# Kernel tuning notes

Measured on AMD Instinct MI355X. Metric: run time of the kernel, lower is better.

## Reference

```python
import jax, jax.numpy as jnp
import numpy as np

BETA = 0.25  # commitment-loss weight (kwargs['beta'])


def setup_inputs() -> dict:
    key = jax.random.key(0)
    k1, k2 = jax.random.split(key)
    B, C, H, W = 16, 256, 64, 64
    K = 2048
    feats = jax.random.normal(k1, (B, C, H, W), dtype=jnp.float32)
    # nn.Embedding init: uniform(-1/n_codewords, 1/codeword_dim)
    codebook = jax.random.uniform(k2, (K, C), minval=-1.0 / K, maxval=1.0 / C,
                                  dtype=jnp.float32)
    return {"feats": feats, "codebook": codebook}


def reference(feats, codebook):
    B, C, H, W = feats.shape
    K = codebook.shape[0]
    z = jnp.transpose(feats, (0, 2, 3, 1))          # [B,H,W,C]
    zf = z.reshape(-1, C)                            # [N,C], N=B*H*W
    # squared-euclidean distances via ||z||^2 + ||e||^2 - 2 z.e : [N,K]
    d = (jnp.sum(zf * zf, axis=1, keepdims=True)
         + jnp.sum(codebook * codebook, axis=1)
         - 2.0 * (zf @ codebook.T))
    min_encoding_indices = jnp.argmin(d, axis=1)     # [N]
    mat_id_probs = jax.nn.softmax(-jnp.abs(d), axis=1)  # [N,K]
    z_q = codebook[min_encoding_indices].reshape(z.shape)  # [B,H,W,C]
    loss = (BETA * jnp.mean((jax.lax.stop_gradient(z_q) - z) ** 2)
            + jnp.mean((z_q - jax.lax.stop_gradient(z)) ** 2))
    # straight-through estimator
    z_q_st = z + jax.lax.stop_gradient(z_q - z)
    z_q_out = jnp.transpose(z_q_st, (0, 3, 1, 2))    # [B,C,H,W]
    idx_out = min_encoding_indices.reshape(B, H, W)
    probs_out = jnp.transpose(mat_id_probs.reshape(B, H, W, K), (0, 3, 1, 2))
    return z_q_out, idx_out, loss, probs_out
```

## Files before the change

### kernel.cpp

```cpp
#include <hip/hip_runtime.h>

#define HW 4096
#define CC 256
#define KK 2048
#define BB 16
#define NN (BB*HW)
#define RPB 128

#define ZQ_SZ   (BB*CC*HW)
#define IDX_OFF ZQ_SZ
#define LOSS_OFF (IDX_OFF + NN)
#define PROBS_OFF (LOSS_OFF + 1)

#define EH_OFF 0
#define EE_OFF 262144
#define ZZ_OFF 264192

#define TAU 0.01f
#define CAND_CAP 512
#define KTC 64
#define KT_N 32

typedef short bf16x8 __attribute__((ext_vector_type(8)));
typedef float f32x16 __attribute__((ext_vector_type(16)));
typedef unsigned int u32;

__device__ __forceinline__ void gload16(const void* g, void* l){
  __builtin_amdgcn_global_load_lds(
      (const __attribute__((address_space(1))) u32*)g,
      (__attribute__((address_space(3))) u32*)l, 16, 0, 0);
}

__device__ __forceinline__ unsigned short bf16rn(float x){
  unsigned u = __float_as_uint(x);
  return (unsigned short)((u + 0x7fffu + ((u >> 16) & 1u)) >> 16);
}

template<int STRIDE>
__device__ __forceinline__ float np_sumsq256(const float* __restrict__ a){
  float res0 = 0.f, res1 = 0.f;
  #pragma unroll
  for (int h = 0; h < 2; h++){
    const float* p = a + (size_t)h * 128 * STRIDE;
    float r[8];
    #pragma unroll
    for (int j = 0; j < 8; j++){ float x = p[(size_t)j * STRIDE]; r[j] = __fmul_rn(x, x); }
    for (int i = 8; i < 128; i += 8){
      #pragma unroll
      for (int j = 0; j < 8; j++){
        float x = p[(size_t)(i + j) * STRIDE];
        r[j] = __fadd_rn(r[j], __fmul_rn(x, x));
      }
    }
    float s = __fadd_rn(__fadd_rn(__fadd_rn(r[0], r[1]), __fadd_rn(r[2], r[3])),
                        __fadd_rn(__fadd_rn(r[4], r[5]), __fadd_rn(r[6], r[7])));
    if (h == 0) res0 = s; else res1 = s;
  }
  return __fadd_rn(res0, res1);
}

__global__ void k_prep2(const float* __restrict__ cb, float* __restrict__ out){
  const int k = blockIdx.x * 256 + threadIdx.x;
  unsigned short* eh = (unsigned short*)(out + EH_OFF);
  const float* row = cb + (size_t)k * CC;
  for (int c = 0; c < CC; c++) eh[k * CC + c] = bf16rn(row[c]);
  out[EE_OFF + k] = np_sumsq256<1>(row);
}

__global__ void k_zz(const float* __restrict__ feats, float* __restrict__ out){
  const int n = blockIdx.x * 256 + threadIdx.x;
  const int b = n >> 12, hw = n & 4095;
  out[ZZ_OFF + n] = np_sumsq256<HW>(feats + (size_t)b * CC * HW + hw);
}

__global__ __launch_bounds__(256, 2)
void k_mfma(const float* __restrict__ feats, const float* __restrict__ cb,
            float* __restrict__ out){
  __shared__ __align__(16) unsigned char lds_e[2][32768];
  __shared__ float ee_lds[KK];
  __shared__ unsigned long long rowkey[RPB];
  __shared__ int cand[CAND_CAP];
  __shared__ int cand_n;
  __shared__ float lsum;

  const int t = threadIdx.x;
  const int w = t >> 6, l = t & 63;
  const int grp = l >> 5;
  const int lane31 = l & 31;
  const int n0 = blockIdx.x * RPB;
  const int bi = n0 >> 12;
  const int hw0 = n0 & 4095;
  const int myhw = hw0 + w * 32 + lane31;

  for (int i = t; i < KK; i += 256) ee_lds[i] = out[EE_OFF + i];
  if (t < RPB) rowkey[t] = ~0ull;
  if (t == 0){ cand_n = 0; lsum = 0.f; }

  bf16x8 ah0[16];
  {
    const float* zb = feats + (size_t)bi * CC * HW + myhw;
    #pragma unroll
    for (int cs = 0; cs < 16; ++cs){
      #pragma unroll
      for (int j = 0; j < 8; ++j)
        ah0[cs][j] = (short)bf16rn(zb[(size_t)(cs * 16 + grp * 8 + j) * HW]);
    }
  }

  const unsigned short* ehg = (const unsigned short*)(out + EH_OFF);

  int ofs_[8];
  #pragma unroll
  for (int i = 0; i < 8; ++i){
    int ix = i * 256 + t;
    int cd = ix & 63, g = (ix >> 6) & 1, cs = ix >> 7;
    ofs_[i] = cd * CC + cs * 16 + g * 8;
  }

#define STAGE(KT, B) { \
    const unsigned short* tb_ = ehg + (size_t)(KT) * (KTC * CC); \
    _Pragma("unroll") \
    for (int i_ = 0; i_ < 8; ++i_) \
      gload16(tb_ + ofs_[i_], &lds_e[B][(i_ * 256 + t) * 16]); }

#define COMPUTE(B) { \
    _Pragma("unroll") \
    for (int ii = 0; ii < 16; ++ii){ accA[ii] = 0.f; accB[ii] = 0.f; } \
    _Pragma("unroll") \
    for (int cs = 0; cs < 16; ++cs){ \
      const unsigned char* bp_ = &lds_e[B][(size_t)(cs * 2 + grp) * 1024 + lane31 * 16]; \
      bf16x8 e0_ = *(const bf16x8*)(bp_); \
      bf16x8 e1_ = *(const bf16x8*)(bp_ + 512); \
      accA = __builtin_amdgcn_mfma_f32_32x32x16_bf16(e0_, ah0[cs], accA, 0, 0, 0); \
      accB = __builtin_amdgcn_mfma_f32_32x32x16_bf16(e1_, ah0[cs], accB, 0, 0, 0); \
    } }

  f32x16 accA, accB;
  float m0 = 3e38f, ss0 = 0.f, inv0 = 0.f;

  STAGE(0, 0);
  __syncthreads();

  for (int kt = 0; kt < 2 * KT_N; ++kt){
    const int tt = kt & 31;
    const int buf = kt & 1;
    if (kt < 2 * KT_N - 1) STAGE((kt + 1) & 31, buf ^ 1);
    COMPUTE(buf);
    const int eebase = tt * 64 + 4 * grp;
    if (kt < KT_N){
      #pragma unroll
      for (int r = 0; r < 16; ++r){
        int off = (r & 3) + 8 * (r >> 2);
        float s0 = ee_lds[eebase + off]      - 2.f * accA[r];
        float s1 = ee_lds[eebase + off + 32] - 2.f * accB[r];
        m0 = fminf(m0, fminf(s0, s1));
        ss0 += __expf(-s0) + __expf(-s1);
      }
      if (kt == KT_N - 1){
        m0 = fminf(m0, __shfl_xor(m0, 32));
        ss0 += __shfl_xor(ss0, 32);
        inv0 = 1.f / ss0;
      }
    } else {
      float* pb = out + (size_t)PROBS_OFF
                + (size_t)(bi * KK + eebase) * HW + myhw;
      #pragma unroll
      for (int r = 0; r < 16; ++r){
        int off = (r & 3) + 8 * (r >> 2);
        float s0 = ee_lds[eebase + off]      - 2.f * accA[r];
        float s1 = ee_lds[eebase + off + 32] - 2.f * accB[r];
        float* p = pb + (size_t)off * HW;
        p[0]               = __expf(-s0) * inv0;
        p[(size_t)32 * HW] = __expf(-s1) * inv0;
        int cg = eebase + off;
        if (s0 <= m0 + TAU){
          int sl = atomicAdd(&cand_n, 1);
          if (sl < CAND_CAP) cand[sl] = ((w * 32 + lane31) << 16) | cg;
        }
        if (s1 <= m0 + TAU){
          int sl = atomicAdd(&cand_n, 1);
          if (sl < CAND_CAP) cand[sl] = ((w * 32 + lane31) << 16) | (cg + 32);
        }
      }
    }
    __syncthreads();
  }

  int nc = cand_n; if (nc > CAND_CAP) nc = CAND_CAP;
  for (int i = t; i < nc; i += 256){
    int rc = cand[i];
    int rl = rc >> 16, code = rc & 0xffff;
    int n = n0 + rl;
    const float* zp = feats + (size_t)(n >> 12) * CC * HW + (n & 4095);
    const float* ep = cb + (size_t)code * CC;
    float a = 0.f;
    #pragma unroll 8
    for (int c = 0; c < CC; ++c) a = __builtin_fmaf(zp[(size_t)c * HW], ep[c], a);
    float t1 = __fadd_rn(out[ZZ_OFF + n], ee_lds[code]);
    float d = __fadd_rn(t1, -2.f * a);
    unsigned long long key = ((unsigned long long)__float_as_uint(d) << 32) | (unsigned)code;
    atomicMin(&rowkey[rl], key);
  }
  __syncthreads();

  if (t < RPB) out[IDX_OFF + n0 + t] = (float)(int)(rowkey[t] & 0xffffffffu);

  if (t < RPB){
    int code = (int)(rowkey[t] & 0xffffffffu);
    const float* ep = cb + (size_t)code * CC;
    const float* zp = feats + (size_t)bi * CC * HW + hw0 + t;
    float s = 0.f;
    for (int c = 0; c < CC; ++c){
      float dz = ep[c] - zp[(size_t)c * HW];
      s = __builtin_fmaf(dz, dz, s);
    }
    atomicAdd(&lsum, s);
  }
  __syncthreads();
  if (t == 0) atomicAdd(out + LOSS_OFF, lsum * (1.25f / 16777216.f));
}

__global__ void k_zq(const float* __restrict__ cb, float* __restrict__ out){
  const int f4 = blockIdx.x * 256 + threadIdx.x;
  const int f = f4 * 4;
  const int b = f >> 20;
  const int rem = f & 1048575;
  const int c = rem >> 12;
  const int hw = rem & 4095;
  const int n = b * HW + hw;
  const float* idxf = out + IDX_OFF;
  float4 iv = *(const float4*)(idxf + n);
  float4 o;
  o.x = cb[(size_t)((int)iv.x) * CC + c];
  o.y = cb[(size_t)((int)iv.y) * CC + c];
  o.z = cb[(size_t)((int)iv.z) * CC + c];
  o.w = cb[(size_t)((int)iv.w) * CC + c];
  *(float4*)(out + f) = o;
}

extern "C" void kernel_launch(void* const* d_in, const int* in_sizes, int n_in,
                              void* d_out, int out_size, void* d_ws, size_t ws_size,
                              hipStream_t stream){
  const float* feats = (const float*)d_in[0];
  const float* cb    = (const float*)d_in[1];
  float* out = (float*)d_out;

  (void)hipMemsetAsync(out + LOSS_OFF, 0, sizeof(float), stream);
  hipLaunchKernelGGL(k_prep2, dim3(8),     dim3(256), 0, stream, cb, out);
  hipLaunchKernelGGL(k_zz,    dim3(256),   dim3(256), 0, stream, feats, out);
  hipLaunchKernelGGL(k_mfma,  dim3(512),   dim3(256), 0, stream, feats, cb, out);
  hipLaunchKernelGGL(k_zq,    dim3(16384), dim3(256), 0, stream, cb, out);
}
```

Measured before the change: 488.8 us.

## Fold codebook norms into MFMA via augmented K-slice, halve tile, raise occupancy

Precomputes -0.5*||e||^2 as a bf16 extra column and appends a 17th MFMA step with a ones vector, so the distance offset comes out of the matrix accumulator instead of being added from an LDS table. The code tile is halved to 32 codes, so each tile now splits its channel range across two accumulators that are summed at the end. The LDS footprint shrinks and launch bounds go from 2 to 4 blocks per CU to raise occupancy. The trade-offs are bf16 rounding of the norm term, which can shift softmax values and candidate selection, twice as many loop iterations each with its own barrier, and register pressure under the tighter launch bound.

New measurement: 534.8 us. 1.09x slower.

```diff
diff --git a/kernel.cpp b/kernel.cpp
--- a/kernel.cpp
+++ b/kernel.cpp
@@ -14,12 +14,14 @@
 
 #define EH_OFF 0
 #define EE_OFF 262144
-#define ZZ_OFF 264192
+#define EXT_OFF 264192
+#define ZZ_OFF 280576
 
 #define TAU 0.01f
 #define CAND_CAP 512
-#define KTC 64
-#define KT_N 32
+#define KTC 32
+#define KT_N 64
+#define CS_N 17
 
 typedef short bf16x8 __attribute__((ext_vector_type(8)));
 typedef float f32x16 __attribute__((ext_vector_type(16)));
@@ -62,9 +64,14 @@
 __global__ void k_prep2(const float* __restrict__ cb, float* __restrict__ out){
   const int k = blockIdx.x * 256 + threadIdx.x;
   unsigned short* eh = (unsigned short*)(out + EH_OFF);
+  unsigned short* ex = (unsigned short*)(out + EXT_OFF);
   const float* row = cb + (size_t)k * CC;
   for (int c = 0; c < CC; c++) eh[k * CC + c] = bf16rn(row[c]);
-  out[EE_OFF + k] = np_sumsq256<1>(row);
+  float ee = np_sumsq256<1>(row);
+  out[EE_OFF + k] = ee;
+  ex[k * 16] = bf16rn(-0.5f * ee);
+  #pragma unroll
+  for (int j = 1; j < 16; ++j) ex[k * 16 + j] = 0;
 }
 
 __global__ void k_zz(const float* __restrict__ feats, float* __restrict__ out){
@@ -73,11 +80,10 @@
   out[ZZ_OFF + n] = np_sumsq256<HW>(feats + (size_t)b * CC * HW + hw);
 }
 
-__global__ __launch_bounds__(256, 2)
+__global__ __launch_bounds__(256, 4)
 void k_mfma(const float* __restrict__ feats, const float* __restrict__ cb,
             float* __restrict__ out){
-  __shared__ __align__(16) unsigned char lds_e[2][32768];
-  __shared__ float ee_lds[KK];
+  __shared__ __align__(16) unsigned char lds_e[2][CS_N * 2 * KTC * 16];
   __shared__ unsigned long long rowkey[RPB];
   __shared__ int cand[CAND_CAP];
   __shared__ int cand_n;
@@ -92,11 +98,10 @@
   const int hw0 = n0 & 4095;
   const int myhw = hw0 + w * 32 + lane31;
 
-  for (int i = t; i < KK; i += 256) ee_lds[i] = out[EE_OFF + i];
   if (t < RPB) rowkey[t] = ~0ull;
   if (t == 0){ cand_n = 0; lsum = 0.f; }
 
-  bf16x8 ah0[16];
+  bf16x8 ah0[16], ahx;
   {
     const float* zb = feats + (size_t)bi * CC * HW + myhw;
     #pragma unroll
@@ -105,34 +110,47 @@
       for (int j = 0; j < 8; ++j)
         ah0[cs][j] = (short)bf16rn(zb[(size_t)(cs * 16 + grp * 8 + j) * HW]);
     }
+    #pragma unroll
+    for (int j = 0; j < 8; ++j) ahx[j] = 0;
+    if (grp == 0) ahx[0] = (short)0x3F80;
   }
 
   const unsigned short* ehg = (const unsigned short*)(out + EH_OFF);
-
-  int ofs_[8];
+  const unsigned short* exg = (const unsigned short*)(out + EXT_OFF);
+
+  int ofs_[4];
   #pragma unroll
-  for (int i = 0; i < 8; ++i){
+  for (int i = 0; i < 4; ++i){
     int ix = i * 256 + t;
-    int cd = ix & 63, g = (ix >> 6) & 1, cs = ix >> 7;
+    int cd = ix & 31, g = (ix >> 5) & 1, cs = ix >> 6;
     ofs_[i] = cd * CC + cs * 16 + g * 8;
   }
 
 #define STAGE(KT, B) { \
     const unsigned short* tb_ = ehg + (size_t)(KT) * (KTC * CC); \
     _Pragma("unroll") \
-    for (int i_ = 0; i_ < 8; ++i_) \
-      gload16(tb_ + ofs_[i_], &lds_e[B][(i_ * 256 + t) * 16]); }
+    for (int i_ = 0; i_ < 4; ++i_) \
+      gload16(tb_ + ofs_[i_], &lds_e[B][(i_ * 256 + t) * 16]); \
+    if (t < 64){ \
+      int cd_ = t & 31, g_ = (t >> 5) & 1; \
+      gload16(exg + ((size_t)((KT) * KTC + cd_) * 16 + g_ * 8), \
+              &lds_e[B][(1024 + t) * 16]); \
+    } }
 
 #define COMPUTE(B) { \
     _Pragma("unroll") \
     for (int ii = 0; ii < 16; ++ii){ accA[ii] = 0.f; accB[ii] = 0.f; } \
     _Pragma("unroll") \
     for (int cs = 0; cs < 16; ++cs){ \
-      const unsigned char* bp_ = &lds_e[B][(size_t)(cs * 2 + grp) * 1024 + lane31 * 16]; \
-      bf16x8 e0_ = *(const bf16x8*)(bp_); \
-      bf16x8 e1_ = *(const bf16x8*)(bp_ + 512); \
-      accA = __builtin_amdgcn_mfma_f32_32x32x16_bf16(e0_, ah0[cs], accA, 0, 0, 0); \
-      accB = __builtin_amdgcn_mfma_f32_32x32x16_bf16(e1_, ah0[cs], accB, 0, 0, 0); \
+      const unsigned char* bp_ = &lds_e[B][(size_t)(cs * 2 + grp) * 512 + lane31 * 16]; \
+      bf16x8 e_ = *(const bf16x8*)(bp_); \
+      if (cs & 1) accB = __builtin_amdgcn_mfma_f32_32x32x16_bf16(e_, ah0[cs], accB, 0, 0, 0); \
+      else        accA = __builtin_amdgcn_mfma_f32_32x32x16_bf16(e_, ah0[cs], accA, 0, 0, 0); \
+    } \
+    { \
+      const unsigned char* bp_ = &lds_e[B][(size_t)(16 * 2 + grp) * 512 + lane31 * 16]; \
+      bf16x8 e_ = *(const bf16x8*)(bp_); \
+      accA = __builtin_amdgcn_mfma_f32_32x32x16_bf16(e_, ahx, accA, 0, 0, 0); \
     } }
 
   f32x16 accA, accB;
@@ -142,19 +160,16 @@
   __syncthreads();
 
   for (int kt = 0; kt < 2 * KT_N; ++kt){
-    const int tt = kt & 31;
+    const int tt = kt & 63;
     const int buf = kt & 1;
-    if (kt < 2 * KT_N - 1) STAGE((kt + 1) & 31, buf ^ 1);
+    if (kt < 2 * KT_N - 1) STAGE((kt + 1) & 63, buf ^ 1);
     COMPUTE(buf);
-    const int eebase = tt * 64 + 4 * grp;
     if (kt < KT_N){
       #pragma unroll
       for (int r = 0; r < 16; ++r){
-        int off = (r & 3) + 8 * (r >> 2);
-        float s0 = ee_lds[eebase + off]      - 2.f * accA[r];
-        float s1 = ee_lds[eebase + off + 32] - 2.f * accB[r];
-        m0 = fminf(m0, fminf(s0, s1));
-        ss0 += __expf(-s0) + __expf(-s1);
+        float s = -2.f * (accA[r] + accB[r]);
+        m0 = fminf(m0, s);
+        ss0 += __expf(-s);
       }
       if (kt == KT_N - 1){
         m0 = fminf(m0, __shfl_xor(m0, 32));
@@ -163,23 +178,16 @@
       }
     } else {
       float* pb = out + (size_t)PROBS_OFF
-                + (size_t)(bi * KK + eebase) * HW + myhw;
+                + (size_t)(bi * KK + tt * KTC + 4 * grp) * HW + myhw;
       #pragma unroll
       for (int r = 0; r < 16; ++r){
         int off = (r & 3) + 8 * (r >> 2);
-        float s0 = ee_lds[eebase + off]      - 2.f * accA[r];
-        float s1 = ee_lds[eebase + off + 32] - 2.f * accB[r];
-        float* p = pb + (size_t)off * HW;
-        p[0]               = __expf(-s0) * inv0;
-        p[(size_t)32 * HW] = __expf(-s1) * inv0;
-        int cg = eebase + off;
-        if (s0 <= m0 + TAU){
+        float s = -2.f * (accA[r] + accB[r]);
+        pb[(size_t)off * HW] = __expf(-s) * inv0;
+        if (s <= m0 + TAU){
           int sl = atomicAdd(&cand_n, 1);
-          if (sl < CAND_CAP) cand[sl] = ((w * 32 + lane31) << 16) | cg;
-        }
-        if (s1 <= m0 + TAU){
-          int sl = atomicAdd(&cand_n, 1);
-          if (sl < CAND_CAP) cand[sl] = ((w * 32 + lane31) << 16) | (cg + 32);
+          if (sl < CAND_CAP)
+            cand[sl] = ((w * 32 + lane31) << 16) | (tt * KTC + 4 * grp + off);
         }
       }
     }
@@ -196,7 +204,7 @@
     float a = 0.f;
     #pragma unroll 8
     for (int c = 0; c < CC; ++c) a = __builtin_fmaf(zp[(size_t)c * HW], ep[c], a);
-    float t1 = __fadd_rn(out[ZZ_OFF + n], ee_lds[code]);
+    float t1 = __fadd_rn(out[ZZ_OFF + n], out[EE_OFF + code]);
     float d = __fadd_rn(t1, -2.f * a);
     unsigned long long key = ((unsigned long long)__float_as_uint(d) << 32) | (unsigned)code;
     atomicMin(&rowkey[rl], key);
```

## Software-pipeline MFMA loop with ping-pong accumulators; parallelize codebook bf16 conversion

Applied to the files above, without the earlier changes.

The main loop is unrolled by two, with two accumulator sets, so the exp and probability-store post-processing of the previous tile runs alongside the MFMAs of the current tile. The codebook bf16 conversion moves from 8 blocks of 2048 serial threads to 256 blocks doing vectorized 16-byte writes. The separate ||z||^2 kernel is removed, and the norm is now computed only for candidate rows during refinement. The cost is more register pressure from the extra accumulators and repeated strided feature reads for each candidate.

After: 460.6 us (median of 2 runs). 5.8% less time.

```diff
diff --git a/kernel.cpp b/kernel.cpp
--- a/kernel.cpp
+++ b/kernel.cpp
@@ -14,7 +14,6 @@
 
 #define EH_OFF 0
 #define EE_OFF 262144
-#define ZZ_OFF 264192
 
 #define TAU 0.01f
 #define CAND_CAP 512
@@ -24,6 +23,7 @@
 typedef short bf16x8 __attribute__((ext_vector_type(8)));
 typedef float f32x16 __attribute__((ext_vector_type(16)));
 typedef unsigned int u32;
+typedef unsigned long long u64;
 
 __device__ __forceinline__ void gload16(const void* g, void* l){
   __builtin_amdgcn_global_load_lds(
@@ -59,18 +59,19 @@
   return __fadd_rn(res0, res1);
 }
 
-__global__ void k_prep2(const float* __restrict__ cb, float* __restrict__ out){
+__global__ void k_cvt(const float* __restrict__ cb, float* __restrict__ out){
+  const int i = blockIdx.x * 256 + threadIdx.x;
+  const int k = i >> 5, c8 = (i & 31) * 8;
+  const float* row = cb + (size_t)k * CC + c8;
+  unsigned short v[8];
+  #pragma unroll
+  for (int j = 0; j < 8; ++j) v[j] = bf16rn(row[j]);
+  *(uint4*)((unsigned short*)(out + EH_OFF) + (size_t)k * CC + c8) = *(uint4*)v;
+}
+
+__global__ void k_ee(const float* __restrict__ cb, float* __restrict__ out){
   const int k = blockIdx.x * 256 + threadIdx.x;
-  unsigned short* eh = (unsigned short*)(out + EH_OFF);
-  const float* row = cb + (size_t)k * CC;
-  for (int c = 0; c < CC; c++) eh[k * CC + c] = bf16rn(row[c]);
-  out[EE_OFF + k] = np_sumsq256<1>(row);
-}
-
-__global__ void k_zz(const float* __restrict__ feats, float* __restrict__ out){
-  const int n = blockIdx.x * 256 + threadIdx.x;
-  const int b = n >> 12, hw = n & 4095;
-  out[ZZ_OFF + n] = np_sumsq256<HW>(feats + (size_t)b * CC * HW + hw);
+  out[EE_OFF + k] = np_sumsq256<1>(cb + (size_t)k * CC);
 }
 
 __global__ __launch_bounds__(256, 2)
@@ -123,90 +124,105 @@
     for (int i_ = 0; i_ < 8; ++i_) \
       gload16(tb_ + ofs_[i_], &lds_e[B][(i_ * 256 + t) * 16]); }
 
-#define COMPUTE(B) { \
+#define COMPUTE(B, AA, AB) { \
     _Pragma("unroll") \
-    for (int ii = 0; ii < 16; ++ii){ accA[ii] = 0.f; accB[ii] = 0.f; } \
+    for (int ii = 0; ii < 16; ++ii){ AA[ii] = 0.f; AB[ii] = 0.f; } \
     _Pragma("unroll") \
     for (int cs = 0; cs < 16; ++cs){ \
       const unsigned char* bp_ = &lds_e[B][(size_t)(cs * 2 + grp) * 1024 + lane31 * 16]; \
       bf16x8 e0_ = *(const bf16x8*)(bp_); \
       bf16x8 e1_ = *(const bf16x8*)(bp_ + 512); \
-      accA = __builtin_amdgcn_mfma_f32_32x32x16_bf16(e0_, ah0[cs], accA, 0, 0, 0); \
-      accB = __builtin_amdgcn_mfma_f32_32x32x16_bf16(e1_, ah0[cs], accB, 0, 0, 0); \
+      AA = __builtin_amdgcn_mfma_f32_32x32x16_bf16(e0_, ah0[cs], AA, 0, 0, 0); \
+      AB = __builtin_amdgcn_mfma_f32_32x32x16_bf16(e1_, ah0[cs], AB, 0, 0, 0); \
     } }
 
-  f32x16 accA, accB;
+#define POST(PKT, PA, PB_) { \
+    const int ptt = (PKT) & 31; \
+    const int eebase = ptt * 64 + 4 * grp; \
+    if ((PKT) < KT_N){ \
+      _Pragma("unroll") \
+      for (int r = 0; r < 16; ++r){ \
+        int off = (r & 3) + 8 * (r >> 2); \
+        float s0 = ee_lds[eebase + off]      - 2.f * PA[r]; \
+        float s1 = ee_lds[eebase + off + 32] - 2.f * PB_[r]; \
+        m0 = fminf(m0, fminf(s0, s1)); \
+        ss0 += __expf(-s0) + __expf(-s1); \
+      } \
+    } else { \
+      float* pb = out + (size_t)PROBS_OFF \
+                + (size_t)(bi * KK + ptt * 64 + 4 * grp) * HW + myhw; \
+      _Pragma("unroll") \
+      for (int r = 0; r < 16; ++r){ \
+        int off = (r & 3) + 8 * (r >> 2); \
+        float s0 = ee_lds[eebase + off]      - 2.f * PA[r]; \
+        float s1 = ee_lds[eebase + off + 32] - 2.f * PB_[r]; \
+        float* p = pb + (size_t)off * HW; \
+        p[0]               = __expf(-s0) * inv0; \
+        p[(size_t)32 * HW] = __expf(-s1) * inv0; \
+        int cg = eebase + off; \
+        if (s0 <= m0 + TAU){ \
+          int sl = atomicAdd(&cand_n, 1); \
+          if (sl < CAND_CAP) cand[sl] = ((w * 32 + lane31) << 16) | cg; \
+        } \
+        if (s1 <= m0 + TAU){ \
+          int sl = atomicAdd(&cand_n, 1); \
+          if (sl < CAND_CAP) cand[sl] = ((w * 32 + lane31) << 16) | (cg + 32); \
+        } \
+      } \
+    } }
+
+  f32x16 aA0, aB0, aA1, aB1;
   float m0 = 3e38f, ss0 = 0.f, inv0 = 0.f;
 
   STAGE(0, 0);
   __syncthreads();
 
-  for (int kt = 0; kt < 2 * KT_N; ++kt){
-    const int tt = kt & 31;
-    const int buf = kt & 1;
-    if (kt < 2 * KT_N - 1) STAGE((kt + 1) & 31, buf ^ 1);
-    COMPUTE(buf);
-    const int eebase = tt * 64 + 4 * grp;
-    if (kt < KT_N){
-      #pragma unroll
-      for (int r = 0; r < 16; ++r){
-        int off = (r & 3) + 8 * (r >> 2);
-        float s0 = ee_lds[eebase + off]      - 2.f * accA[r];
-        float s1 = ee_lds[eebase + off + 32] - 2.f * accB[r];
-        m0 = fminf(m0, fminf(s0, s1));
-        ss0 += __expf(-s0) + __expf(-s1);
-      }
-      if (kt == KT_N - 1){
+  for (int kt2 = 0; kt2 < KT_N; ++kt2){
+    const int ktA = 2 * kt2;
+    {
+      STAGE((ktA + 1) & 31, 1);
+      if (ktA > 0) POST(ktA - 1, aA1, aB1);
+      if (ktA == KT_N){
         m0 = fminf(m0, __shfl_xor(m0, 32));
         ss0 += __shfl_xor(ss0, 32);
         inv0 = 1.f / ss0;
       }
-    } else {
-      float* pb = out + (size_t)PROBS_OFF
-                + (size_t)(bi * KK + eebase) * HW + myhw;
-      #pragma unroll
-      for (int r = 0; r < 16; ++r){
-        int off = (r & 3) + 8 * (r >> 2);
-        float s0 = ee_lds[eebase + off]      - 2.f * accA[r];
-        float s1 = ee_lds[eebase + off + 32] - 2.f * accB[r];
-        float* p = pb + (size_t)off * HW;
-        p[0]               = __expf(-s0) * inv0;
-        p[(size_t)32 * HW] = __expf(-s1) * inv0;
-        int cg = eebase + off;
-        if (s0 <= m0 + TAU){
-          int sl = atomicAdd(&cand_n, 1);
-          if (sl < CAND_CAP) cand[sl] = ((w * 32 + lane31) << 16) | cg;
-        }
-        if (s1 <= m0 + TAU){
-          int sl = atomicAdd(&cand_n, 1);
-          if (sl < CAND_CAP) cand[sl] = ((w * 32 + lane31) << 16) | (cg + 32);
-        }
-      }
-    }
-    __syncthreads();
-  }
+      COMPUTE(0, aA0, aB0);
+      __syncthreads();
+    }
+    {
+      const int ktB = ktA + 1;
+      if (ktB < 2 * KT_N - 1) STAGE((ktB + 1) & 31, 0);
+      POST(ktB - 1, aA0, aB0);
+      COMPUTE(1, aA1, aB1);
+      __syncthreads();
+    }
+  }
+  POST(2 * KT_N - 1, aA1, aB1);
+  __syncthreads();
 
   int nc = cand_n; if (nc > CAND_CAP) nc = CAND_CAP;
   for (int i = t; i < nc; i += 256){
     int rc = cand[i];
-    int rl = rc >> 16, code = rc & 0xffff;
+    int rl = (rc >> 16) & 127, code = rc & 2047;
     int n = n0 + rl;
     const float* zp = feats + (size_t)(n >> 12) * CC * HW + (n & 4095);
     const float* ep = cb + (size_t)code * CC;
     float a = 0.f;
     #pragma unroll 8
     for (int c = 0; c < CC; ++c) a = __builtin_fmaf(zp[(size_t)c * HW], ep[c], a);
-    float t1 = __fadd_rn(out[ZZ_OFF + n], ee_lds[code]);
+    float zzv = np_sumsq256<HW>(zp);
+    float t1 = __fadd_rn(zzv, ee_lds[code]);
     float d = __fadd_rn(t1, -2.f * a);
     unsigned long long key = ((unsigned long long)__float_as_uint(d) << 32) | (unsigned)code;
     atomicMin(&rowkey[rl], key);
   }
   __syncthreads();
 
-  if (t < RPB) out[IDX_OFF + n0 + t] = (float)(int)(rowkey[t] & 0xffffffffu);
+  if (t < RPB) out[IDX_OFF + n0 + t] = (float)(int)(rowkey[t] & 2047u);
 
   if (t < RPB){
-    int code = (int)(rowkey[t] & 0xffffffffu);
+    int code = (int)(rowkey[t] & 2047u);
     const float* ep = cb + (size_t)code * CC;
     const float* zp = feats + (size_t)bi * CC * HW + hw0 + t;
     float s = 0.f;
@@ -246,8 +262,8 @@
   float* out = (float*)d_out;
 
   (void)hipMemsetAsync(out + LOSS_OFF, 0, sizeof(float), stream);
-  hipLaunchKernelGGL(k_prep2, dim3(8),     dim3(256), 0, stream, cb, out);
-  hipLaunchKernelGGL(k_zz,    dim3(256),   dim3(256), 0, stream, feats, out);
-  hipLaunchKernelGGL(k_mfma,  dim3(512),   dim3(256), 0, stream, feats, cb, out);
-  hipLaunchKernelGGL(k_zq,    dim3(16384), dim3(256), 0, stream, cb, out);
-}
+  hipLaunchKernelGGL(k_cvt,  dim3(256),   dim3(256), 0, stream, cb, out);
+  hipLaunchKernelGGL(k_ee,   dim3(8),     dim3(256), 0, stream, cb, out);
+  hipLaunchKernelGGL(k_mfma, dim3(512),   dim3(256), 0, stream, feats, cb, out);
+  hipLaunchKernelGGL(k_zq,   dim3(16384), dim3(256), 0, stream, cb, out);
+}
```
